# Kernel optimization log

Measured on AMD Instinct MI355X. Metric: run time of the kernel, lower is better.

## Reference

```python
import jax, jax.numpy as jnp
import numpy as np

N_NODES = 50000
N_EDGES = 800000
D = 64


def setup_inputs() -> dict:
    key = jax.random.key(0)
    ks = jax.random.split(key, 8)
    x = jax.random.normal(ks[0], (N_NODES, D), dtype=jnp.float32)
    src = jax.random.randint(ks[1], (N_EDGES,), 0, N_NODES, dtype=jnp.int32)
    dst = jax.random.randint(ks[2], (N_EDGES,), 0, N_NODES, dtype=jnp.int32)
    s = 1.0 / np.sqrt(D)
    w1_0 = jax.random.uniform(ks[3], (D, D), jnp.float32, -s, s)
    w2_0 = jax.random.uniform(ks[4], (D, D), jnp.float32, -s, s)
    w1_1 = jax.random.uniform(ks[5], (D, D), jnp.float32, -s, s)
    w2_1 = jax.random.uniform(ks[6], (D, D), jnp.float32, -s, s)
    b = jnp.zeros((D,), jnp.float32)
    return {"x": x, "src": src, "dst": dst,
            "w1_0": w1_0, "b1_0": b, "w2_0": w2_0, "b2_0": b,
            "w1_1": w1_1, "b1_1": b, "w2_1": w2_1, "b2_1": b}


def _gin_layer(x, src, dst, w1, b1, w2, b2):
    # sum aggregation over edges: agg[i] = sum_{(j->i) in E} x[j]
    agg = jax.ops.segment_sum(x[src], dst, num_segments=N_NODES)
    h = x + agg  # (1 + eps) * x + agg, eps = 0 (DGL GINConv default)
    h = jnp.tanh(h @ w1 + b1)
    return h @ w2 + b2


def reference(x, src, dst, w1_0, b1_0, w2_0, b2_0, w1_1, b1_1, w2_1, b2_1):
    x = _gin_layer(x, src, dst, w1_0, b1_0, w2_0, b2_0)
    x = _gin_layer(x, src, dst, w1_1, b1_1, w2_1, b2_1)
    return x
```

## Files before the change

### kernel.cpp

```cpp
#include <hip/hip_runtime.h>

#define D 64
#define CAP 56

typedef __attribute__((ext_vector_type(8))) short short8;
typedef __attribute__((ext_vector_type(4))) float f32x4;

__device__ __forceinline__ unsigned short f2bf(float f) {
    unsigned u = __float_as_uint(f);
    u = (u + 0x7fff + ((u >> 16) & 1)) >> 16;
    return (unsigned short)u;
}
__device__ __forceinline__ float bf_lo(unsigned u) { return __uint_as_float(u << 16); }
__device__ __forceinline__ float bf_hi(unsigned u) { return __uint_as_float(u & 0xffff0000u); }

__global__ __launch_bounds__(256) void prep_scatter_kernel(
    const int* __restrict__ src, const int* __restrict__ dst,
    int* __restrict__ deg, unsigned short* __restrict__ buf, int n_edges, int nsb,
    const float* __restrict__ x, unsigned short* __restrict__ xb, int n4, int ncb,
    const float* __restrict__ w1_0, const float* __restrict__ w2_0,
    const float* __restrict__ w1_1, const float* __restrict__ w2_1,
    unsigned short* __restrict__ wt)
{
    const int b = blockIdx.x;
    if (b < nsb) {
        int e = b * 256 + threadIdx.x;
        if (e < n_edges) {
            int d = dst[e];
            int p = atomicAdd(&deg[d], 1);
            if (p < CAP) buf[(size_t)d * CAP + p] = (unsigned short)src[e];
        }
    } else if (b < nsb + ncb) {
        int i = (b - nsb) * 256 + threadIdx.x;
        if (i < n4) {
            float4 v = *(const float4*)(x + i * 4);
            ushort4 o;
            o.x = f2bf(v.x); o.y = f2bf(v.y); o.z = f2bf(v.z); o.w = f2bf(v.w);
            *(ushort4*)(xb + i * 4) = o;
        }
    } else {
        int i = (b - nsb - ncb) * 256 + threadIdx.x;
        int m = i >> 12, r = i & 4095;
        int n = r >> 6, k = r & 63;
        const float* w = (m == 0) ? w1_0 : (m == 1) ? w2_0 : (m == 2) ? w1_1 : w2_1;
        wt[i] = f2bf(w[k * 64 + n]);
    }
}

template <bool WRITE_BF16>
__global__ __launch_bounds__(256) void gin_fused_mfma(
    const unsigned short* __restrict__ hb, int n_nodes,
    const int* __restrict__ deg, const unsigned short* __restrict__ buf,
    const unsigned short* __restrict__ w1t, const float* __restrict__ b1,
    const unsigned short* __restrict__ w2t, const float* __restrict__ b2,
    float* __restrict__ out_f, unsigned short* __restrict__ out_b)
{
    __shared__ unsigned short sh [64][72];
    __shared__ unsigned short st [64][72];
    __shared__ unsigned short sw1[64][72];
    __shared__ unsigned short sw2[64][72];
    __shared__ __align__(16) unsigned short sidx[64][56];
    __shared__ int sdeg[64];

    const int t    = threadIdx.x;
    const int lane = t & 63;
    const int wave = t >> 6;
    const int nb   = blockIdx.x * 64;

    {
        const uint4* gsrc = (const uint4*)(buf + (size_t)nb * CAP);
        uint4* ldst = (uint4*)&sidx[0][0];
        for (int i = t; i < 448; i += 256) ldst[i] = gsrc[i];
    }
    if (t < 64) {
        int gn = nb + t;
        int dd = (gn < n_nodes) ? deg[gn] : 0;
        sdeg[t] = dd < CAP ? dd : CAP;
    }
    for (int c = t; c < 512; c += 256) {
        int row = c >> 3, c8 = (c & 7) << 3;
        int gn = nb + row; if (gn >= n_nodes) gn = n_nodes - 1;
        *(uint4*)&sh [row][c8] = *(const uint4*)(hb  + (size_t)gn * D + c8);
        *(uint4*)&sw1[row][c8] = *(const uint4*)(w1t + row * D + c8);
        *(uint4*)&sw2[row][c8] = *(const uint4*)(w2t + row * D + c8);
    }
    __syncthreads();

    const int q  = lane >> 3;
    const int fc = (lane & 7) << 3;

    #pragma unroll
    for (int p = 0; p < 2; ++p) {
        const int m = 16 * wave + (p << 3) + q;
        uint4 u = *(const uint4*)&sh[m][fc];
        float a0 = bf_lo(u.x), a1 = bf_hi(u.x), a2 = bf_lo(u.y), a3 = bf_hi(u.y);
        float a4 = bf_lo(u.z), a5 = bf_hi(u.z), a6 = bf_lo(u.w), a7 = bf_hi(u.w);
        const int dd = sdeg[m];
        const unsigned short* ip = sidx[m];
        int j = 0;
        for (; j + 4 <= dd; j += 4) {
            int s0 = ip[j], s1 = ip[j + 1], s2 = ip[j + 2], s3 = ip[j + 3];
            uint4 v0 = *(const uint4*)(hb + (size_t)s0 * D + fc);
            uint4 v1 = *(const uint4*)(hb + (size_t)s1 * D + fc);
            uint4 v2 = *(const uint4*)(hb + (size_t)s2 * D + fc);
            uint4 v3 = *(const uint4*)(hb + (size_t)s3 * D + fc);
            a0 += bf_lo(v0.x) + bf_lo(v1.x) + bf_lo(v2.x) + bf_lo(v3.x);
            a1 += bf_hi(v0.x) + bf_hi(v1.x) + bf_hi(v2.x) + bf_hi(v3.x);
            a2 += bf_lo(v0.y) + bf_lo(v1.y) + bf_lo(v2.y) + bf_lo(v3.y);
            a3 += bf_hi(v0.y) + bf_hi(v1.y) + bf_hi(v2.y) + bf_hi(v3.y);
            a4 += bf_lo(v0.z) + bf_lo(v1.z) + bf_lo(v2.z) + bf_lo(v3.z);
            a5 += bf_hi(v0.z) + bf_hi(v1.z) + bf_hi(v2.z) + bf_hi(v3.z);
            a6 += bf_lo(v0.w) + bf_lo(v1.w) + bf_lo(v2.w) + bf_lo(v3.w);
            a7 += bf_hi(v0.w) + bf_hi(v1.w) + bf_hi(v2.w) + bf_hi(v3.w);
        }
        for (; j < dd; ++j) {
            int s = ip[j];
            uint4 v = *(const uint4*)(hb + (size_t)s * D + fc);
            a0 += bf_lo(v.x); a1 += bf_hi(v.x);
            a2 += bf_lo(v.y); a3 += bf_hi(v.y);
            a4 += bf_lo(v.z); a5 += bf_hi(v.z);
            a6 += bf_lo(v.w); a7 += bf_hi(v.w);
        }
        uint4 o;
        o.x = (unsigned)f2bf(a0) | ((unsigned)f2bf(a1) << 16);
        o.y = (unsigned)f2bf(a2) | ((unsigned)f2bf(a3) << 16);
        o.z = (unsigned)f2bf(a4) | ((unsigned)f2bf(a5) << 16);
        o.w = (unsigned)f2bf(a6) | ((unsigned)f2bf(a7) << 16);
        *(uint4*)&sh[m][fc] = o;
    }

    const int quad = lane >> 4;
    const int col  = lane & 15;
    const int arow = 16 * wave + col;
    const int koff = quad << 3;

    short8 a0 = *(const short8*)&sh[arow][koff];
    short8 a1 = *(const short8*)&sh[arow][32 + koff];

    #pragma unroll
    for (int nt = 0; nt < 4; ++nt) {
        int n = (nt << 4) + col;
        short8 bw0 = *(const short8*)&sw1[n][koff];
        short8 bw1 = *(const short8*)&sw1[n][32 + koff];
        float bv = b1[n];
        f32x4 c = {bv, bv, bv, bv};
        c = __builtin_amdgcn_mfma_f32_16x16x32_bf16(a0, bw0, c, 0, 0, 0);
        c = __builtin_amdgcn_mfma_f32_16x16x32_bf16(a1, bw1, c, 0, 0, 0);
        #pragma unroll
        for (int r = 0; r < 4; ++r)
            st[16 * wave + (quad << 2) + r][n] = f2bf(tanhf(c[r]));
    }

    short8 p0 = *(const short8*)&st[arow][koff];
    short8 p1 = *(const short8*)&st[arow][32 + koff];

    #pragma unroll
    for (int nt = 0; nt < 4; ++nt) {
        int n = (nt << 4) + col;
        short8 bw0 = *(const short8*)&sw2[n][koff];
        short8 bw1 = *(const short8*)&sw2[n][32 + koff];
        float bv = b2[n];
        f32x4 c = {bv, bv, bv, bv};
        c = __builtin_amdgcn_mfma_f32_16x16x32_bf16(p0, bw0, c, 0, 0, 0);
        c = __builtin_amdgcn_mfma_f32_16x16x32_bf16(p1, bw1, c, 0, 0, 0);
        #pragma unroll
        for (int r = 0; r < 4; ++r) {
            int row = nb + 16 * wave + (quad << 2) + r;
            if (WRITE_BF16) {
                out_b[(size_t)row * D + n] = f2bf(c[r]);
            } else if (row < n_nodes) {
                out_f[(size_t)row * D + n] = c[r];
            }
        }
    }
}

extern "C" void kernel_launch(void* const* d_in, const int* in_sizes, int n_in,
                              void* d_out, int out_size, void* d_ws, size_t ws_size,
                              hipStream_t stream)
{
    const float* x    = (const float*)d_in[0];
    const int*   src  = (const int*)  d_in[1];
    const int*   dst  = (const int*)  d_in[2];
    const float* w1_0 = (const float*)d_in[3];
    const float* b1_0 = (const float*)d_in[4];
    const float* w2_0 = (const float*)d_in[5];
    const float* b2_0 = (const float*)d_in[6];
    const float* w1_1 = (const float*)d_in[7];
    const float* b1_1 = (const float*)d_in[8];
    const float* w2_1 = (const float*)d_in[9];
    const float* b2_1 = (const float*)d_in[10];
    float* out = (float*)d_out;

    const int n_nodes = in_sizes[0] / D;
    const int n_edges = in_sizes[1];
    const int n_pad   = (n_nodes + 63) & ~63;

    int*            deg = (int*)d_ws;
    unsigned short* buf = (unsigned short*)(deg + n_nodes);
    unsigned short* xb  = buf + (size_t)n_nodes * CAP;
    unsigned short* x1b = xb  + (size_t)n_pad * D;
    unsigned short* wt  = x1b + (size_t)n_pad * D;

    const int n4  = n_nodes * D / 4;
    const int nsb = (n_edges + 255) / 256;
    const int ncb = (n4 + 255) / 256;

    hipMemsetAsync(deg, 0, (size_t)n_nodes * sizeof(int) + (size_t)n_nodes * CAP * sizeof(unsigned short), stream);
    prep_scatter_kernel<<<nsb + ncb + 64, 256, 0, stream>>>(
        src, dst, deg, buf, n_edges, nsb,
        x, xb, n4, ncb,
        w1_0, w2_0, w1_1, w2_1, wt);

    const int fused_blocks = n_pad / 64;

    gin_fused_mfma<true><<<fused_blocks, 256, 0, stream>>>(
        xb, n_nodes, deg, buf, wt, b1_0, wt + 4096, b2_0, nullptr, x1b);
    gin_fused_mfma<false><<<fused_blocks, 256, 0, stream>>>(
        x1b, n_nodes, deg, buf, wt + 8192, b1_1, wt + 12288, b2_1, out, nullptr);
}
```

Baseline: 189.6 us.

## Merge prep and both GIN layers into one persistent kernel with grid barriers

Replaces the scatter/convert kernel and the two per-layer fused kernels with a single persistent launch of 768 blocks. Phases are separated by software grid barriers built on atomic counters. Tiles are processed in a grid-stride loop. The memset now clears only the degree array and barrier counters, not the neighbor buffer. This removes launch gaps and most of the memset traffic, but adds barrier spin cost and relies on all 768 blocks being co-resident.

```diff
diff --git a/kernel.cpp b/kernel.cpp
--- a/kernel.cpp
+++ b/kernel.cpp
@@ -2,6 +2,7 @@
 
 #define D 64
 #define CAP 56
+#define NBLK 768
 
 typedef __attribute__((ext_vector_type(8))) short short8;
 typedef __attribute__((ext_vector_type(4))) float f32x4;
@@ -14,89 +15,72 @@
 __device__ __forceinline__ float bf_lo(unsigned u) { return __uint_as_float(u << 16); }
 __device__ __forceinline__ float bf_hi(unsigned u) { return __uint_as_float(u & 0xffff0000u); }
 
-__global__ __launch_bounds__(256) void prep_scatter_kernel(
-    const int* __restrict__ src, const int* __restrict__ dst,
-    int* __restrict__ deg, unsigned short* __restrict__ buf, int n_edges, int nsb,
-    const float* __restrict__ x, unsigned short* __restrict__ xb, int n4, int ncb,
-    const float* __restrict__ w1_0, const float* __restrict__ w2_0,
-    const float* __restrict__ w1_1, const float* __restrict__ w2_1,
-    unsigned short* __restrict__ wt)
-{
-    const int b = blockIdx.x;
-    if (b < nsb) {
-        int e = b * 256 + threadIdx.x;
-        if (e < n_edges) {
-            int d = dst[e];
-            int p = atomicAdd(&deg[d], 1);
-            if (p < CAP) buf[(size_t)d * CAP + p] = (unsigned short)src[e];
-        }
-    } else if (b < nsb + ncb) {
-        int i = (b - nsb) * 256 + threadIdx.x;
-        if (i < n4) {
-            float4 v = *(const float4*)(x + i * 4);
-            ushort4 o;
-            o.x = f2bf(v.x); o.y = f2bf(v.y); o.z = f2bf(v.z); o.w = f2bf(v.w);
-            *(ushort4*)(xb + i * 4) = o;
-        }
-    } else {
-        int i = (b - nsb - ncb) * 256 + threadIdx.x;
-        int m = i >> 12, r = i & 4095;
-        int n = r >> 6, k = r & 63;
-        const float* w = (m == 0) ? w1_0 : (m == 1) ? w2_0 : (m == 2) ? w1_1 : w2_1;
-        wt[i] = f2bf(w[k * 64 + n]);
-    }
-}
+__device__ __forceinline__ void gridbar(int* cnt) {
+    __syncthreads();
+    if (threadIdx.x == 0) {
+        __threadfence();
+        __hip_atomic_fetch_add(cnt, 1, __ATOMIC_ACQ_REL, __HIP_MEMORY_SCOPE_AGENT);
+        while (__hip_atomic_load(cnt, __ATOMIC_ACQUIRE, __HIP_MEMORY_SCOPE_AGENT) < NBLK)
+            __builtin_amdgcn_s_sleep(8);
+    }
+    __syncthreads();
+    __threadfence();
+}
+
+struct SharedT {
+    unsigned short sh [64][72];
+    unsigned short st [64][72];
+    unsigned short sw1[64][72];
+    unsigned short sw2[64][72];
+    __align__(16) unsigned short sidx[64][56];
+    int sdeg[64];
+};
 
 template <bool WRITE_BF16>
-__global__ __launch_bounds__(256) void gin_fused_mfma(
+__device__ __forceinline__ void layer_tile(
+    SharedT& S, int tile,
     const unsigned short* __restrict__ hb, int n_nodes,
     const int* __restrict__ deg, const unsigned short* __restrict__ buf,
     const unsigned short* __restrict__ w1t, const float* __restrict__ b1,
     const unsigned short* __restrict__ w2t, const float* __restrict__ b2,
     float* __restrict__ out_f, unsigned short* __restrict__ out_b)
 {
-    __shared__ unsigned short sh [64][72];
-    __shared__ unsigned short st [64][72];
-    __shared__ unsigned short sw1[64][72];
-    __shared__ unsigned short sw2[64][72];
-    __shared__ __align__(16) unsigned short sidx[64][56];
-    __shared__ int sdeg[64];
-
     const int t    = threadIdx.x;
     const int lane = t & 63;
     const int wave = t >> 6;
-    const int nb   = blockIdx.x * 64;
+    const int nb   = tile * 64;
+
+    __syncthreads();
 
     {
         const uint4* gsrc = (const uint4*)(buf + (size_t)nb * CAP);
-        uint4* ldst = (uint4*)&sidx[0][0];
+        uint4* ldst = (uint4*)&S.sidx[0][0];
         for (int i = t; i < 448; i += 256) ldst[i] = gsrc[i];
     }
     if (t < 64) {
         int gn = nb + t;
         int dd = (gn < n_nodes) ? deg[gn] : 0;
-        sdeg[t] = dd < CAP ? dd : CAP;
+        S.sdeg[t] = dd < CAP ? dd : CAP;
     }
     for (int c = t; c < 512; c += 256) {
         int row = c >> 3, c8 = (c & 7) << 3;
         int gn = nb + row; if (gn >= n_nodes) gn = n_nodes - 1;
-        *(uint4*)&sh [row][c8] = *(const uint4*)(hb  + (size_t)gn * D + c8);
-        *(uint4*)&sw1[row][c8] = *(const uint4*)(w1t + row * D + c8);
-        *(uint4*)&sw2[row][c8] = *(const uint4*)(w2t + row * D + c8);
+        *(uint4*)&S.sh [row][c8] = *(const uint4*)(hb  + (size_t)gn * D + c8);
+        *(uint4*)&S.sw1[row][c8] = *(const uint4*)(w1t + row * D + c8);
+        *(uint4*)&S.sw2[row][c8] = *(const uint4*)(w2t + row * D + c8);
     }
     __syncthreads();
 
     const int q  = lane >> 3;
     const int fc = (lane & 7) << 3;
-
     #pragma unroll
     for (int p = 0; p < 2; ++p) {
         const int m = 16 * wave + (p << 3) + q;
-        uint4 u = *(const uint4*)&sh[m][fc];
+        uint4 u = *(const uint4*)&S.sh[m][fc];
         float a0 = bf_lo(u.x), a1 = bf_hi(u.x), a2 = bf_lo(u.y), a3 = bf_hi(u.y);
         float a4 = bf_lo(u.z), a5 = bf_hi(u.z), a6 = bf_lo(u.w), a7 = bf_hi(u.w);
-        const int dd = sdeg[m];
-        const unsigned short* ip = sidx[m];
+        const int dd = S.sdeg[m];
+        const unsigned short* ip = S.sidx[m];
         int j = 0;
         for (; j + 4 <= dd; j += 4) {
             int s0 = ip[j], s1 = ip[j + 1], s2 = ip[j + 2], s3 = ip[j + 3];
@@ -126,7 +110,7 @@
         o.y = (unsigned)f2bf(a2) | ((unsigned)f2bf(a3) << 16);
         o.z = (unsigned)f2bf(a4) | ((unsigned)f2bf(a5) << 16);
         o.w = (unsigned)f2bf(a6) | ((unsigned)f2bf(a7) << 16);
-        *(uint4*)&sh[m][fc] = o;
+        *(uint4*)&S.sh[m][fc] = o;
     }
 
     const int quad = lane >> 4;
@@ -134,31 +118,31 @@
     const int arow = 16 * wave + col;
     const int koff = quad << 3;
 
-    short8 a0 = *(const short8*)&sh[arow][koff];
-    short8 a1 = *(const short8*)&sh[arow][32 + koff];
+    short8 a0 = *(const short8*)&S.sh[arow][koff];
+    short8 a1 = *(const short8*)&S.sh[arow][32 + koff];
 
     #pragma unroll
     for (int nt = 0; nt < 4; ++nt) {
         int n = (nt << 4) + col;
-        short8 bw0 = *(const short8*)&sw1[n][koff];
-        short8 bw1 = *(const short8*)&sw1[n][32 + koff];
+        short8 bw0 = *(const short8*)&S.sw1[n][koff];
+        short8 bw1 = *(const short8*)&S.sw1[n][32 + koff];
         float bv = b1[n];
         f32x4 c = {bv, bv, bv, bv};
         c = __builtin_amdgcn_mfma_f32_16x16x32_bf16(a0, bw0, c, 0, 0, 0);
         c = __builtin_amdgcn_mfma_f32_16x16x32_bf16(a1, bw1, c, 0, 0, 0);
         #pragma unroll
         for (int r = 0; r < 4; ++r)
-            st[16 * wave + (quad << 2) + r][n] = f2bf(tanhf(c[r]));
-    }
-
-    short8 p0 = *(const short8*)&st[arow][koff];
-    short8 p1 = *(const short8*)&st[arow][32 + koff];
+            S.st[16 * wave + (quad << 2) + r][n] = f2bf(tanhf(c[r]));
+    }
+
+    short8 p0 = *(const short8*)&S.st[arow][koff];
+    short8 p1 = *(const short8*)&S.st[arow][32 + koff];
 
     #pragma unroll
     for (int nt = 0; nt < 4; ++nt) {
         int n = (nt << 4) + col;
-        short8 bw0 = *(const short8*)&sw2[n][koff];
-        short8 bw1 = *(const short8*)&sw2[n][32 + koff];
+        short8 bw0 = *(const short8*)&S.sw2[n][koff];
+        short8 bw1 = *(const short8*)&S.sw2[n][32 + koff];
         float bv = b2[n];
         f32x4 c = {bv, bv, bv, bv};
         c = __builtin_amdgcn_mfma_f32_16x16x32_bf16(p0, bw0, c, 0, 0, 0);
@@ -173,6 +157,59 @@
             }
         }
     }
+}
+
+__global__ __launch_bounds__(256, 3) void gin_mega(
+    const int* __restrict__ src, const int* __restrict__ dst, int n_edges,
+    const float* __restrict__ x, int n_nodes, int n_tiles,
+    const float* __restrict__ w1_0, const float* __restrict__ b1_0,
+    const float* __restrict__ w2_0, const float* __restrict__ b2_0,
+    const float* __restrict__ w1_1, const float* __restrict__ b1_1,
+    const float* __restrict__ w2_1, const float* __restrict__ b2_1,
+    int* __restrict__ deg, int* __restrict__ cnt,
+    unsigned short* __restrict__ buf, unsigned short* __restrict__ xb,
+    unsigned short* __restrict__ x1b, unsigned short* __restrict__ wt,
+    float* __restrict__ out)
+{
+    __shared__ SharedT S;
+    const int b = blockIdx.x;
+    const int t = threadIdx.x;
+
+    {
+        const int EPB = (n_edges + NBLK - 1) / NBLK;
+        int e0 = b * EPB, e1 = min(e0 + EPB, n_edges);
+        for (int e = e0 + t; e < e1; e += 256) {
+            int d = dst[e];
+            int p = atomicAdd(&deg[d], 1);
+            if (p < CAP) buf[(size_t)d * CAP + p] = (unsigned short)src[e];
+        }
+        const int n4 = n_nodes * D / 4;
+        const int CPB = (n4 + NBLK - 1) / NBLK;
+        int i0 = b * CPB, i1 = min(i0 + CPB, n4);
+        for (int i = i0 + t; i < i1; i += 256) {
+            float4 v = *(const float4*)(x + i * 4);
+            ushort4 o;
+            o.x = f2bf(v.x); o.y = f2bf(v.y); o.z = f2bf(v.z); o.w = f2bf(v.w);
+            *(ushort4*)(xb + i * 4) = o;
+        }
+        if (b < 64) {
+            int i = b * 256 + t;
+            int m = i >> 12, r = i & 4095;
+            int n = r >> 6, k = r & 63;
+            const float* w = (m == 0) ? w1_0 : (m == 1) ? w2_0 : (m == 2) ? w1_1 : w2_1;
+            wt[i] = f2bf(w[k * 64 + n]);
+        }
+    }
+    gridbar(cnt + 0);
+
+    for (int tile = b; tile < n_tiles; tile += NBLK)
+        layer_tile<true>(S, tile, xb, n_nodes, deg, buf,
+                         wt, b1_0, wt + 4096, b2_0, nullptr, x1b);
+    gridbar(cnt + 1);
+
+    for (int tile = b; tile < n_tiles; tile += NBLK)
+        layer_tile<false>(S, tile, x1b, n_nodes, deg, buf,
+                          wt + 8192, b1_1, wt + 12288, b2_1, out, nullptr);
 }
 
 extern "C" void kernel_launch(void* const* d_in, const int* in_sizes, int n_in,
@@ -195,27 +232,19 @@
     const int n_nodes = in_sizes[0] / D;
     const int n_edges = in_sizes[1];
     const int n_pad   = (n_nodes + 63) & ~63;
+    const int n_tiles = n_pad / 64;
 
     int*            deg = (int*)d_ws;
-    unsigned short* buf = (unsigned short*)(deg + n_nodes);
+    int*            cnt = deg + n_nodes;
+    unsigned short* buf = (unsigned short*)(cnt + 4);
     unsigned short* xb  = buf + (size_t)n_nodes * CAP;
     unsigned short* x1b = xb  + (size_t)n_pad * D;
     unsigned short* wt  = x1b + (size_t)n_pad * D;
 
-    const int n4  = n_nodes * D / 4;
-    const int nsb = (n_edges + 255) / 256;
-    const int ncb = (n4 + 255) / 256;
-
-    hipMemsetAsync(deg, 0, (size_t)n_nodes * sizeof(int) + (size_t)n_nodes * CAP * sizeof(unsigned short), stream);
-    prep_scatter_kernel<<<nsb + ncb + 64, 256, 0, stream>>>(
-        src, dst, deg, buf, n_edges, nsb,
-        x, xb, n4, ncb,
-        w1_0, w2_0, w1_1, w2_1, wt);
-
-    const int fused_blocks = n_pad / 64;
-
-    gin_fused_mfma<true><<<fused_blocks, 256, 0, stream>>>(
-        xb, n_nodes, deg, buf, wt, b1_0, wt + 4096, b2_0, nullptr, x1b);
-    gin_fused_mfma<false><<<fused_blocks, 256, 0, stream>>>(
-        x1b, n_nodes, deg, buf, wt + 8192, b1_1, wt + 12288, b2_1, out, nullptr);
-}
+    hipMemsetAsync(deg, 0, ((size_t)n_nodes + 4) * sizeof(int), stream);
+
+    gin_mega<<<NBLK, 256, 0, stream>>>(
+        src, dst, n_edges, x, n_nodes, n_tiles,
+        w1_0, b1_0, w2_0, b2_0, w1_1, b1_1, w2_1, b2_1,
+        deg, cnt, buf, xb, x1b, wt, out);
+}
```

New measurement: 525.4 us. 2.77x slower.

## Split features into two half-width planes and gather each half in separate kernels

Applied to the files above, without the earlier changes.

Node features are stored as two 32-column bf16 planes. Each layer's neighbor gather is split into a half-gather kernel that writes fp32 partial sums and a dense kernel that gathers the other half before running the MFMA MLP. The aim is to halve the randomly accessed working set per pass so the gathered table fits better in cache. The cost is extra kernel launches and an fp32 intermediate round trip. The memset also no longer clears the neighbor buffer, which is safe because only entries below the clamped degree are read.

```diff
diff --git a/kernel.cpp b/kernel.cpp
--- a/kernel.cpp
+++ b/kernel.cpp
@@ -1,10 +1,12 @@
 #include <hip/hip_runtime.h>
 
 #define D 64
+#define HD 32
 #define CAP 56
 
 typedef __attribute__((ext_vector_type(8))) short short8;
 typedef __attribute__((ext_vector_type(4))) float f32x4;
+typedef __attribute__((ext_vector_type(4))) float float4v;
 
 __device__ __forceinline__ unsigned short f2bf(float f) {
     unsigned u = __float_as_uint(f);
@@ -17,7 +19,8 @@
 __global__ __launch_bounds__(256) void prep_scatter_kernel(
     const int* __restrict__ src, const int* __restrict__ dst,
     int* __restrict__ deg, unsigned short* __restrict__ buf, int n_edges, int nsb,
-    const float* __restrict__ x, unsigned short* __restrict__ xb, int n4, int ncb,
+    const float* __restrict__ x, unsigned short* __restrict__ x0a,
+    unsigned short* __restrict__ x0b, int n4, int ncb,
     const float* __restrict__ w1_0, const float* __restrict__ w2_0,
     const float* __restrict__ w1_1, const float* __restrict__ w2_1,
     unsigned short* __restrict__ wt)
@@ -36,7 +39,10 @@
             float4 v = *(const float4*)(x + i * 4);
             ushort4 o;
             o.x = f2bf(v.x); o.y = f2bf(v.y); o.z = f2bf(v.z); o.w = f2bf(v.w);
-            *(ushort4*)(xb + i * 4) = o;
+            int n = i >> 4, c = i & 15;
+            unsigned short* p = (c < 8) ? (x0a + (size_t)n * HD + c * 4)
+                                        : (x0b + (size_t)n * HD + (c - 8) * 4);
+            *(ushort4*)p = o;
         }
     } else {
         int i = (b - nsb - ncb) * 256 + threadIdx.x;
@@ -47,13 +53,81 @@
     }
 }
 
+__global__ __launch_bounds__(256) void gather_half_kernel(
+    const unsigned short* __restrict__ xp, const int* __restrict__ deg,
+    const unsigned short* __restrict__ buf, float* __restrict__ acc32, int n_nodes)
+{
+    __shared__ __align__(16) unsigned short sidx[64][56];
+    __shared__ int sdeg[64];
+
+    const int t    = threadIdx.x;
+    const int lane = t & 63;
+    const int wave = t >> 6;
+    const int nb   = blockIdx.x * 64;
+
+    {
+        const uint4* gsrc = (const uint4*)(buf + (size_t)nb * CAP);
+        uint4* ldst = (uint4*)&sidx[0][0];
+        for (int i = t; i < 448; i += 256) ldst[i] = gsrc[i];
+    }
+    if (t < 64) {
+        int gn = nb + t;
+        int dd = (gn < n_nodes) ? deg[gn] : 0;
+        sdeg[t] = dd < CAP ? dd : CAP;
+    }
+    __syncthreads();
+
+    const int q  = lane >> 2;
+    const int ch = (lane & 3) << 3;
+    const int m  = 16 * wave + q;
+    const int node = nb + m;
+
+    uint4 u = *(const uint4*)(xp + (size_t)node * HD + ch);
+    float a0 = bf_lo(u.x), a1 = bf_hi(u.x), a2 = bf_lo(u.y), a3 = bf_hi(u.y);
+    float a4 = bf_lo(u.z), a5 = bf_hi(u.z), a6 = bf_lo(u.w), a7 = bf_hi(u.w);
+
+    const int dd = sdeg[m];
+    const unsigned short* ip = sidx[m];
+    int j = 0;
+    for (; j + 4 <= dd; j += 4) {
+        int s0 = ip[j], s1 = ip[j + 1], s2 = ip[j + 2], s3 = ip[j + 3];
+        uint4 v0 = *(const uint4*)(xp + (size_t)s0 * HD + ch);
+        uint4 v1 = *(const uint4*)(xp + (size_t)s1 * HD + ch);
+        uint4 v2 = *(const uint4*)(xp + (size_t)s2 * HD + ch);
+        uint4 v3 = *(const uint4*)(xp + (size_t)s3 * HD + ch);
+        a0 += bf_lo(v0.x) + bf_lo(v1.x) + bf_lo(v2.x) + bf_lo(v3.x);
+        a1 += bf_hi(v0.x) + bf_hi(v1.x) + bf_hi(v2.x) + bf_hi(v3.x);
+        a2 += bf_lo(v0.y) + bf_lo(v1.y) + bf_lo(v2.y) + bf_lo(v3.y);
+        a3 += bf_hi(v0.y) + bf_hi(v1.y) + bf_hi(v2.y) + bf_hi(v3.y);
+        a4 += bf_lo(v0.z) + bf_lo(v1.z) + bf_lo(v2.z) + bf_lo(v3.z);
+        a5 += bf_hi(v0.z) + bf_hi(v1.z) + bf_hi(v2.z) + bf_hi(v3.z);
+        a6 += bf_lo(v0.w) + bf_lo(v1.w) + bf_lo(v2.w) + bf_lo(v3.w);
+        a7 += bf_hi(v0.w) + bf_hi(v1.w) + bf_hi(v2.w) + bf_hi(v3.w);
+    }
+    for (; j < dd; ++j) {
+        int s = ip[j];
+        uint4 v = *(const uint4*)(xp + (size_t)s * HD + ch);
+        a0 += bf_lo(v.x); a1 += bf_hi(v.x);
+        a2 += bf_lo(v.y); a3 += bf_hi(v.y);
+        a4 += bf_lo(v.z); a5 += bf_hi(v.z);
+        a6 += bf_lo(v.w); a7 += bf_hi(v.w);
+    }
+
+    float* ap = acc32 + (size_t)node * HD + ((lane & 3) << 3);
+    float4v o0 = {a0, a1, a2, a3};
+    float4v o1 = {a4, a5, a6, a7};
+    __builtin_nontemporal_store(o0, (float4v*)ap);
+    __builtin_nontemporal_store(o1, (float4v*)(ap + 4));
+}
+
 template <bool WRITE_BF16>
-__global__ __launch_bounds__(256) void gin_fused_mfma(
-    const unsigned short* __restrict__ hb, int n_nodes,
-    const int* __restrict__ deg, const unsigned short* __restrict__ buf,
+__global__ __launch_bounds__(256) void gin_dense_half(
+    const unsigned short* __restrict__ xpB, const float* __restrict__ acc32,
+    int n_nodes, const int* __restrict__ deg, const unsigned short* __restrict__ buf,
     const unsigned short* __restrict__ w1t, const float* __restrict__ b1,
     const unsigned short* __restrict__ w2t, const float* __restrict__ b2,
-    float* __restrict__ out_f, unsigned short* __restrict__ out_b)
+    float* __restrict__ out_f, unsigned short* __restrict__ o_pA,
+    unsigned short* __restrict__ o_pB)
 {
     __shared__ unsigned short sh [64][72];
     __shared__ unsigned short st [64][72];
@@ -77,33 +151,40 @@
         int dd = (gn < n_nodes) ? deg[gn] : 0;
         sdeg[t] = dd < CAP ? dd : CAP;
     }
-    for (int c = t; c < 512; c += 256) {
-        int row = c >> 3, c8 = (c & 7) << 3;
-        int gn = nb + row; if (gn >= n_nodes) gn = n_nodes - 1;
-        *(uint4*)&sh [row][c8] = *(const uint4*)(hb  + (size_t)gn * D + c8);
+    for (int i = t; i < 512; i += 256) {
+        int row = i >> 3, c8 = (i & 7) << 3;
         *(uint4*)&sw1[row][c8] = *(const uint4*)(w1t + row * D + c8);
         *(uint4*)&sw2[row][c8] = *(const uint4*)(w2t + row * D + c8);
     }
+    for (int i = t; i < 512; i += 256) {
+        int row = i >> 3, c = (i & 7) << 2;
+        float4v v = __builtin_nontemporal_load(
+            (const float4v*)(acc32 + (size_t)(nb + row) * HD + c));
+        ushort4 o;
+        o.x = f2bf(v.x); o.y = f2bf(v.y); o.z = f2bf(v.z); o.w = f2bf(v.w);
+        *(ushort4*)&sh[row][c] = o;
+    }
     __syncthreads();
 
-    const int q  = lane >> 3;
-    const int fc = (lane & 7) << 3;
-
-    #pragma unroll
-    for (int p = 0; p < 2; ++p) {
-        const int m = 16 * wave + (p << 3) + q;
-        uint4 u = *(const uint4*)&sh[m][fc];
+    {
+        const int q  = lane >> 2;
+        const int ch = (lane & 3) << 3;
+        const int m  = 16 * wave + q;
+        const int node = nb + m;
+
+        uint4 u = *(const uint4*)(xpB + (size_t)node * HD + ch);
         float a0 = bf_lo(u.x), a1 = bf_hi(u.x), a2 = bf_lo(u.y), a3 = bf_hi(u.y);
         float a4 = bf_lo(u.z), a5 = bf_hi(u.z), a6 = bf_lo(u.w), a7 = bf_hi(u.w);
+
         const int dd = sdeg[m];
         const unsigned short* ip = sidx[m];
         int j = 0;
         for (; j + 4 <= dd; j += 4) {
             int s0 = ip[j], s1 = ip[j + 1], s2 = ip[j + 2], s3 = ip[j + 3];
-            uint4 v0 = *(const uint4*)(hb + (size_t)s0 * D + fc);
-            uint4 v1 = *(const uint4*)(hb + (size_t)s1 * D + fc);
-            uint4 v2 = *(const uint4*)(hb + (size_t)s2 * D + fc);
-            uint4 v3 = *(const uint4*)(hb + (size_t)s3 * D + fc);
+            uint4 v0 = *(const uint4*)(xpB + (size_t)s0 * HD + ch);
+            uint4 v1 = *(const uint4*)(xpB + (size_t)s1 * HD + ch);
+            uint4 v2 = *(const uint4*)(xpB + (size_t)s2 * HD + ch);
+            uint4 v3 = *(const uint4*)(xpB + (size_t)s3 * HD + ch);
             a0 += bf_lo(v0.x) + bf_lo(v1.x) + bf_lo(v2.x) + bf_lo(v3.x);
             a1 += bf_hi(v0.x) + bf_hi(v1.x) + bf_hi(v2.x) + bf_hi(v3.x);
             a2 += bf_lo(v0.y) + bf_lo(v1.y) + bf_lo(v2.y) + bf_lo(v3.y);
@@ -115,18 +196,17 @@
         }
         for (; j < dd; ++j) {
             int s = ip[j];
-            uint4 v = *(const uint4*)(hb + (size_t)s * D + fc);
+            uint4 v = *(const uint4*)(xpB + (size_t)s * HD + ch);
             a0 += bf_lo(v.x); a1 += bf_hi(v.x);
             a2 += bf_lo(v.y); a3 += bf_hi(v.y);
             a4 += bf_lo(v.z); a5 += bf_hi(v.z);
             a6 += bf_lo(v.w); a7 += bf_hi(v.w);
         }
-        uint4 o;
-        o.x = (unsigned)f2bf(a0) | ((unsigned)f2bf(a1) << 16);
-        o.y = (unsigned)f2bf(a2) | ((unsigned)f2bf(a3) << 16);
-        o.z = (unsigned)f2bf(a4) | ((unsigned)f2bf(a5) << 16);
-        o.w = (unsigned)f2bf(a6) | ((unsigned)f2bf(a7) << 16);
-        *(uint4*)&sh[m][fc] = o;
+        ushort4 oA, oB;
+        oA.x = f2bf(a0); oA.y = f2bf(a1); oA.z = f2bf(a2); oA.w = f2bf(a3);
+        oB.x = f2bf(a4); oB.y = f2bf(a5); oB.z = f2bf(a6); oB.w = f2bf(a7);
+        *(ushort4*)&sh[m][32 + ch]     = oA;
+        *(ushort4*)&sh[m][32 + ch + 4] = oB;
     }
 
     const int quad = lane >> 4;
@@ -167,7 +247,8 @@
         for (int r = 0; r < 4; ++r) {
             int row = nb + 16 * wave + (quad << 2) + r;
             if (WRITE_BF16) {
-                out_b[(size_t)row * D + n] = f2bf(c[r]);
+                if (n < HD) o_pA[(size_t)row * HD + n]        = f2bf(c[r]);
+                else        o_pB[(size_t)row * HD + (n - HD)] = f2bf(c[r]);
             } else if (row < n_nodes) {
                 out_f[(size_t)row * D + n] = c[r];
             }
@@ -195,27 +276,31 @@
     const int n_nodes = in_sizes[0] / D;
     const int n_edges = in_sizes[1];
     const int n_pad   = (n_nodes + 63) & ~63;
-
-    int*            deg = (int*)d_ws;
-    unsigned short* buf = (unsigned short*)(deg + n_nodes);
-    unsigned short* xb  = buf + (size_t)n_nodes * CAP;
-    unsigned short* x1b = xb  + (size_t)n_pad * D;
-    unsigned short* wt  = x1b + (size_t)n_pad * D;
+    const int n_tiles = n_pad / 64;
+
+    int*            deg  = (int*)d_ws;
+    unsigned short* buf  = (unsigned short*)(deg + n_nodes);
+    unsigned short* x0a  = buf + (size_t)n_nodes * CAP;
+    unsigned short* x0b  = x0a + (size_t)n_pad * HD;
+    unsigned short* x1a  = x0b + (size_t)n_pad * HD;
+    unsigned short* x1b  = x1a + (size_t)n_pad * HD;
+    unsigned short* wt   = x1b + (size_t)n_pad * HD;
+    float*          acc32 = (float*)(wt + 4 * 64 * 64);
 
     const int n4  = n_nodes * D / 4;
     const int nsb = (n_edges + 255) / 256;
     const int ncb = (n4 + 255) / 256;
 
-    hipMemsetAsync(deg, 0, (size_t)n_nodes * sizeof(int) + (size_t)n_nodes * CAP * sizeof(unsigned short), stream);
+    hipMemsetAsync(deg, 0, (size_t)n_nodes * sizeof(int), stream);
     prep_scatter_kernel<<<nsb + ncb + 64, 256, 0, stream>>>(
         src, dst, deg, buf, n_edges, nsb,
-        x, xb, n4, ncb,
+        x, x0a, x0b, n4, ncb,
         w1_0, w2_0, w1_1, w2_1, wt);
 
-    const int fused_blocks = n_pad / 64;
-
-    gin_fused_mfma<true><<<fused_blocks, 256, 0, stream>>>(
-        xb, n_nodes, deg, buf, wt, b1_0, wt + 4096, b2_0, nullptr, x1b);
-    gin_fused_mfma<false><<<fused_blocks, 256, 0, stream>>>(
-        x1b, n_nodes, deg, buf, wt + 8192, b1_1, wt + 12288, b2_1, out, nullptr);
-}
+    gather_half_kernel<<<n_tiles, 256, 0, stream>>>(x0a, deg, buf, acc32, n_nodes);
+    gin_dense_half<true><<<n_tiles, 256, 0, stream>>>(
+        x0b, acc32, n_nodes, deg, buf, wt, b1_0, wt + 4096, b2_0, nullptr, x1a, x1b);
+    gather_half_kernel<<<n_tiles, 256, 0, stream>>>(x1a, deg, buf, acc32, n_nodes);
+    gin_dense_half<false><<<n_tiles, 256, 0, stream>>>(
+        x1b, acc32, n_nodes, deg, buf, wt + 8192, b1_1, wt + 12288, b2_1, out, nullptr, nullptr);
+}
```

Measured after the change: 193.1 us. Within noise of the previous version (+1.8%).
